# Optimization experiments

Measured on AMD Instinct MI355X. Metric: run time of the kernel, lower is better.

## Reference

```python
import jax, jax.numpy as jnp
import numpy as np

N_NODES = 50000
N_EDGES = 625000
D_FEAT = 128


def setup_inputs() -> dict:
    key = jax.random.key(0)
    k1, k2, k3, k4 = jax.random.split(key, 4)
    h = jax.random.normal(k1, (N_NODES, D_FEAT), dtype=jnp.float32)
    w = jax.random.uniform(k2, (N_EDGES, 1), dtype=jnp.float32)
    src = jax.random.randint(k3, (N_EDGES,), 0, N_NODES, dtype=jnp.int32)
    dst = jax.random.randint(k4, (N_EDGES,), 0, N_NODES, dtype=jnp.int32)
    return {"h": h, "w": w, "src": src, "dst": dst, "mode": 1}


def reference(h, w, src, dst, mode):
    # h: [N, D] node features; w: [E, 1] edge weights; src/dst: [E] edge list.
    n = h.shape[0]
    if mode == 1:  # 'polar': m = h[src] * w, sum to dst  (edge-weighted SpMM)
        msg = h[src] * w  # [E, D]
        out = jax.ops.segment_sum(msg, dst, num_segments=n)
    else:  # GCN symmetric normalization: D^{-1/2} A D^{-1/2} h (out-degree based)
        deg = jax.ops.segment_sum(jnp.ones(src.shape[0], dtype=h.dtype), src,
                                  num_segments=n)
        norm = jnp.power(deg, -0.5)[:, None]  # [N, 1]
        feat = h * norm
        out = jax.ops.segment_sum(feat[src], dst, num_segments=n)
        out = norm * out
    return out
```

## Files before the change

### kernel.cpp

```cpp
#include <hip/hip_runtime.h>
#include <hip/hip_fp16.h>

#define D_FEAT 128


__device__ __forceinline__ unsigned wq16(float f) {
    int q = (int)(f * 65536.0f);
    if (q < 0) q = 0;
    if (q > 65535) q = 65535;
    return (unsigned)q;
}

__device__ __forceinline__ unsigned h2u(__half2 v) {
    union { __half2 h; unsigned u; } cv; cv.h = v; return cv.u;
}
__device__ __forceinline__ float2 u2f2(unsigned u) {
    union { unsigned u; __half2 h; } cv; cv.u = u;
    return __half22float2(cv.h);
}

__global__ void bucket_conv_kernel(const float* __restrict__ h,
                                   const int* __restrict__ src, const int* __restrict__ dst,
                                   const float* __restrict__ w,
                                   int* __restrict__ cursor, float* __restrict__ deg,
                                   int* __restrict__ ovfcnt, int* __restrict__ ovf,
                                   unsigned* __restrict__ rec, int cap,
                                   uint4* __restrict__ h16,
                                   int E, int nBucketBlocks, int nGroups8, int cs,
                                   const int* __restrict__ mode) {
    if ((int)blockIdx.x >= nBucketBlocks) {
        int i = (blockIdx.x - nBucketBlocks) * blockDim.x + threadIdx.x;
        if (i >= nGroups8) return;
        const float4* hf4 = (const float4*)h;
        float4 x = hf4[2 * i];
        float4 y = hf4[2 * i + 1];
        uint4 o;
        o.x = h2u(__float22half2_rn(make_float2(x.x, x.y)));
        o.y = h2u(__float22half2_rn(make_float2(x.z, x.w)));
        o.z = h2u(__float22half2_rn(make_float2(y.x, y.y)));
        o.w = h2u(__float22half2_rn(make_float2(y.z, y.w)));
        h16[i] = o;
        return;
    }
    int e = blockIdx.x * blockDim.x + threadIdx.x;
    if (e >= E) return;
    bool m1 = (*mode == 1);
    int s = src[e];
    int d = dst[e];
    float wv = w[e];
    if (!m1) atomicAdd(&deg[s], 1.0f);
    int pos = atomicAdd(&cursor[(size_t)d * cs], 1);
    unsigned r = ((unsigned)s << 16) | wq16(wv);
    if (pos < cap) rec[(size_t)d * cap + pos] = r;
    else           ovf[atomicAdd(ovfcnt, 1)] = e;
}

__device__ __forceinline__ unsigned bcast_rec(unsigned r0, unsigned r1, int j) {
    unsigned lo = __shfl(r0, j & 31, 32);
    unsigned hi = __shfl(r1, j & 31, 32);
    return (j < 32) ? lo : hi;
}

__global__ void gather4_f16_kernel(const uint2* __restrict__ h16,
                                   const float* __restrict__ hf,
                                   const int* __restrict__ cursor, const float* __restrict__ deg,
                                   const unsigned* __restrict__ rec, int cap,
                                   const int* __restrict__ ovfcnt, const int* __restrict__ ovf,
                                   const int* __restrict__ src, const int* __restrict__ dst,
                                   const float* __restrict__ w,
                                   float* __restrict__ out, int N, int cs,
                                   const int* __restrict__ mode) {
    long long gid = (long long)blockIdx.x * blockDim.x + threadIdx.x;
    int node = (int)(gid >> 5);
    int lane = (int)(gid & 31);
    if (node >= N) return;
    bool m1 = (*mode == 1);
    int cnt = cursor[(size_t)node * cs];
    int inb = cnt < cap ? cnt : cap;
    const unsigned* row = rec + (size_t)node * cap;
    unsigned r0 = (lane < inb) ? row[lane] : 0u;
    unsigned r1 = (lane + 32 < inb) ? row[lane + 32] : 0u;

    float a0 = 0.f, a1 = 0.f, a2 = 0.f, a3 = 0.f;
    float b0 = 0.f, b1 = 0.f, b2 = 0.f, b3 = 0.f;
    float c0 = 0.f, c1 = 0.f, c2 = 0.f, c3 = 0.f;
    float d0 = 0.f, d1 = 0.f, d2 = 0.f, d3 = 0.f;

    int j = 0;
    if (m1) {
        const float Q = 1.52587890625e-05f;
        for (; j + 3 < inb; j += 4) {
            unsigned m0 = bcast_rec(r0, r1, j);
            unsigned m1r = bcast_rec(r0, r1, j + 1);
            unsigned m2r = bcast_rec(r0, r1, j + 2);
            unsigned m3r = bcast_rec(r0, r1, j + 3);
            float sc0 = ((float)(m0 & 0xFFFFu) + 0.5f) * Q;
            float sc1 = ((float)(m1r & 0xFFFFu) + 0.5f) * Q;
            float sc2 = ((float)(m2r & 0xFFFFu) + 0.5f) * Q;
            float sc3 = ((float)(m3r & 0xFFFFu) + 0.5f) * Q;
            uint2 v0 = h16[(size_t)(m0 >> 16) * 32 + lane];
            uint2 v1 = h16[(size_t)(m1r >> 16) * 32 + lane];
            uint2 v2 = h16[(size_t)(m2r >> 16) * 32 + lane];
            uint2 v3 = h16[(size_t)(m3r >> 16) * 32 + lane];
            float2 f0a = u2f2(v0.x), f0b = u2f2(v0.y);
            float2 f1a = u2f2(v1.x), f1b = u2f2(v1.y);
            float2 f2a = u2f2(v2.x), f2b = u2f2(v2.y);
            float2 f3a = u2f2(v3.x), f3b = u2f2(v3.y);
            a0 += f0a.x * sc0; a1 += f0a.y * sc0; a2 += f0b.x * sc0; a3 += f0b.y * sc0;
            b0 += f1a.x * sc1; b1 += f1a.y * sc1; b2 += f1b.x * sc1; b3 += f1b.y * sc1;
            c0 += f2a.x * sc2; c1 += f2a.y * sc2; c2 += f2b.x * sc2; c3 += f2b.y * sc2;
            d0 += f3a.x * sc3; d1 += f3a.y * sc3; d2 += f3b.x * sc3; d3 += f3b.y * sc3;
        }
        for (; j < inb; ++j) {
            unsigned m0 = bcast_rec(r0, r1, j);
            float sc0 = ((float)(m0 & 0xFFFFu) + 0.5f) * Q;
            uint2 v0 = h16[(size_t)(m0 >> 16) * 32 + lane];
            float2 f0a = u2f2(v0.x), f0b = u2f2(v0.y);
            a0 += f0a.x * sc0; a1 += f0a.y * sc0; a2 += f0b.x * sc0; a3 += f0b.y * sc0;
        }
    } else {
        for (; j + 3 < inb; j += 4) {
            unsigned m0 = bcast_rec(r0, r1, j);
            unsigned m1r = bcast_rec(r0, r1, j + 1);
            unsigned m2r = bcast_rec(r0, r1, j + 2);
            unsigned m3r = bcast_rec(r0, r1, j + 3);
            int s0 = (int)(m0 >> 16), s1 = (int)(m1r >> 16);
            int s2 = (int)(m2r >> 16), s3 = (int)(m3r >> 16);
            float sc0 = rsqrtf(deg[s0]);
            float sc1 = rsqrtf(deg[s1]);
            float sc2 = rsqrtf(deg[s2]);
            float sc3 = rsqrtf(deg[s3]);
            uint2 v0 = h16[(size_t)s0 * 32 + lane];
            uint2 v1 = h16[(size_t)s1 * 32 + lane];
            uint2 v2 = h16[(size_t)s2 * 32 + lane];
            uint2 v3 = h16[(size_t)s3 * 32 + lane];
            float2 f0a = u2f2(v0.x), f0b = u2f2(v0.y);
            float2 f1a = u2f2(v1.x), f1b = u2f2(v1.y);
            float2 f2a = u2f2(v2.x), f2b = u2f2(v2.y);
            float2 f3a = u2f2(v3.x), f3b = u2f2(v3.y);
            a0 += f0a.x * sc0; a1 += f0a.y * sc0; a2 += f0b.x * sc0; a3 += f0b.y * sc0;
            b0 += f1a.x * sc1; b1 += f1a.y * sc1; b2 += f1b.x * sc1; b3 += f1b.y * sc1;
            c0 += f2a.x * sc2; c1 += f2a.y * sc2; c2 += f2b.x * sc2; c3 += f2b.y * sc2;
            d0 += f3a.x * sc3; d1 += f3a.y * sc3; d2 += f3b.x * sc3; d3 += f3b.y * sc3;
        }
        for (; j < inb; ++j) {
            unsigned m0 = bcast_rec(r0, r1, j);
            int s0 = (int)(m0 >> 16);
            float sc0 = rsqrtf(deg[s0]);
            uint2 v0 = h16[(size_t)s0 * 32 + lane];
            float2 f0a = u2f2(v0.x), f0b = u2f2(v0.y);
            a0 += f0a.x * sc0; a1 += f0a.y * sc0; a2 += f0b.x * sc0; a3 += f0b.y * sc0;
        }
    }

    a0 += b0 + c0 + d0; a1 += b1 + c1 + d1;
    a2 += b2 + c2 + d2; a3 += b3 + c3 + d3;

    if (cnt > cap) {
        int total = *ovfcnt;
        for (int k = 0; k < total; ++k) {
            int e = ovf[k];
            if (dst[e] == node) {
                int s = src[e];
                float sc = m1 ? w[e] : rsqrtf(deg[s]);
                float4 v = ((const float4*)(hf + (long long)s * D_FEAT))[lane];
                a0 += v.x * sc; a1 += v.y * sc; a2 += v.z * sc; a3 += v.w * sc;
            }
        }
    }
    float fin = m1 ? 1.0f : rsqrtf(deg[node]);
    float4 r; r.x = a0 * fin; r.y = a1 * fin; r.z = a2 * fin; r.w = a3 * fin;
    ((float4*)(out + (long long)node * D_FEAT))[lane] = r;
}


__global__ void bucket_multi_kernel(const int* __restrict__ src, const int* __restrict__ dst,
                                    const float* __restrict__ w,
                                    int* __restrict__ cursor, float* __restrict__ deg,
                                    int* __restrict__ ovfcnt, int* __restrict__ ovf,
                                    unsigned* __restrict__ rec, int cap,
                                    int E, const int* __restrict__ mode) {
    int t = blockIdx.x * blockDim.x + threadIdx.x;
    int base = t * 4;
    if (base >= E) return;
    bool m1 = (*mode == 1);
    if (base + 3 < E) {
        int4   s4 = ((const int4*)src)[t];
        int4   d4 = ((const int4*)dst)[t];
        float4 w4 = ((const float4*)w)[t];
        if (!m1) {
            atomicAdd(&deg[s4.x], 1.0f); atomicAdd(&deg[s4.y], 1.0f);
            atomicAdd(&deg[s4.z], 1.0f); atomicAdd(&deg[s4.w], 1.0f);
        }
        int p0 = atomicAdd(&cursor[d4.x], 1);
        int p1 = atomicAdd(&cursor[d4.y], 1);
        int p2 = atomicAdd(&cursor[d4.z], 1);
        int p3 = atomicAdd(&cursor[d4.w], 1);
        unsigned r0 = ((unsigned)s4.x << 16) | wq16(w4.x);
        unsigned r1 = ((unsigned)s4.y << 16) | wq16(w4.y);
        unsigned r2 = ((unsigned)s4.z << 16) | wq16(w4.z);
        unsigned r3 = ((unsigned)s4.w << 16) | wq16(w4.w);
        if (p0 < cap) rec[(size_t)d4.x * cap + p0] = r0; else ovf[atomicAdd(ovfcnt, 1)] = base + 0;
        if (p1 < cap) rec[(size_t)d4.y * cap + p1] = r1; else ovf[atomicAdd(ovfcnt, 1)] = base + 1;
        if (p2 < cap) rec[(size_t)d4.z * cap + p2] = r2; else ovf[atomicAdd(ovfcnt, 1)] = base + 2;
        if (p3 < cap) rec[(size_t)d4.w * cap + p3] = r3; else ovf[atomicAdd(ovfcnt, 1)] = base + 3;
    } else {
        for (int e = base; e < E; ++e) {
            int s = src[e], d = dst[e];
            if (!m1) atomicAdd(&deg[s], 1.0f);
            int pos = atomicAdd(&cursor[d], 1);
            if (pos < cap) rec[(size_t)d * cap + pos] = ((unsigned)s << 16) | wq16(w[e]);
            else ovf[atomicAdd(ovfcnt, 1)] = e;
        }
    }
}

__global__ void gather4_f32_kernel(const float* __restrict__ h,
                                   const int* __restrict__ cursor, const float* __restrict__ deg,
                                   const unsigned* __restrict__ rec, int cap,
                                   const int* __restrict__ ovfcnt, const int* __restrict__ ovf,
                                   const int* __restrict__ src, const int* __restrict__ dst,
                                   const float* __restrict__ w,
                                   float* __restrict__ out, int N, const int* __restrict__ mode) {
    long long gid = (long long)blockIdx.x * blockDim.x + threadIdx.x;
    int node = (int)(gid >> 5);
    int lane = (int)(gid & 31);
    if (node >= N) return;
    bool m1 = (*mode == 1);
    int cnt = cursor[node];
    int inb = cnt < cap ? cnt : cap;
    const unsigned* row = rec + (size_t)node * cap;
    unsigned r0 = (lane < inb) ? row[lane] : 0u;
    unsigned r1 = (lane + 32 < inb) ? row[lane + 32] : 0u;
    const float4* h4 = (const float4*)h;
    float a0 = 0.f, a1 = 0.f, a2 = 0.f, a3 = 0.f;
    float b0 = 0.f, b1 = 0.f, b2 = 0.f, b3 = 0.f;
    int j = 0;
    const float Q = 1.52587890625e-05f;
    for (; j + 1 < inb; j += 2) {
        unsigned m0 = bcast_rec(r0, r1, j);
        unsigned m1r = bcast_rec(r0, r1, j + 1);
        int s0 = (int)(m0 >> 16), s1 = (int)(m1r >> 16);
        float sc0 = m1 ? ((float)(m0 & 0xFFFFu) + 0.5f) * Q : rsqrtf(deg[s0]);
        float sc1 = m1 ? ((float)(m1r & 0xFFFFu) + 0.5f) * Q : rsqrtf(deg[s1]);
        float4 v0 = h4[(size_t)s0 * 32 + lane];
        float4 v1 = h4[(size_t)s1 * 32 + lane];
        a0 += v0.x * sc0; a1 += v0.y * sc0; a2 += v0.z * sc0; a3 += v0.w * sc0;
        b0 += v1.x * sc1; b1 += v1.y * sc1; b2 += v1.z * sc1; b3 += v1.w * sc1;
    }
    if (j < inb) {
        unsigned m0 = bcast_rec(r0, r1, j);
        int s0 = (int)(m0 >> 16);
        float sc0 = m1 ? ((float)(m0 & 0xFFFFu) + 0.5f) * Q : rsqrtf(deg[s0]);
        float4 v0 = h4[(size_t)s0 * 32 + lane];
        a0 += v0.x * sc0; a1 += v0.y * sc0; a2 += v0.z * sc0; a3 += v0.w * sc0;
    }
    a0 += b0; a1 += b1; a2 += b2; a3 += b3;
    if (cnt > cap) {
        int total = *ovfcnt;
        for (int k = 0; k < total; ++k) {
            int e = ovf[k];
            if (dst[e] == node) {
                int s = src[e];
                float sc = m1 ? w[e] : rsqrtf(deg[s]);
                float4 v = ((const float4*)(h + (long long)s * D_FEAT))[lane];
                a0 += v.x * sc; a1 += v.y * sc; a2 += v.z * sc; a3 += v.w * sc;
            }
        }
    }
    float fin = m1 ? 1.0f : rsqrtf(deg[node]);
    float4 r; r.x = a0 * fin; r.y = a1 * fin; r.z = a2 * fin; r.w = a3 * fin;
    ((float4*)(out + (long long)node * D_FEAT))[lane] = r;
}


__global__ void bucket_direct_kernel(const int* __restrict__ src, const int* __restrict__ dst,
                                     const float* __restrict__ w,
                                     int* __restrict__ cursor, float* __restrict__ deg,
                                     int* __restrict__ ovfcnt, int* __restrict__ ovf,
                                     uint2* __restrict__ epack, int cap,
                                     int E, const int* __restrict__ mode) {
    int e = blockIdx.x * blockDim.x + threadIdx.x;
    if (e >= E) return;
    bool m1 = (*mode == 1);
    int d = dst[e];
    int s = src[e];
    if (!m1) atomicAdd(&deg[s], 1.0f);
    int pos = atomicAdd(&cursor[d], 1);
    if (pos < cap) {
        float sc = m1 ? w[e] : 0.0f;
        epack[(size_t)d * cap + pos] = make_uint2((unsigned)s, __float_as_uint(sc));
    } else {
        ovf[atomicAdd(ovfcnt, 1)] = e;
    }
}

__global__ void gather_cap_kernel(const float* __restrict__ h,
                                  const int* __restrict__ cursor, const float* __restrict__ deg,
                                  const uint2* __restrict__ epack, int cap,
                                  const int* __restrict__ ovfcnt, const int* __restrict__ ovf,
                                  const int* __restrict__ src, const int* __restrict__ dst,
                                  const float* __restrict__ w,
                                  float* __restrict__ out, int N, const int* __restrict__ mode) {
    long long gid = (long long)blockIdx.x * blockDim.x + threadIdx.x;
    int node = (int)(gid >> 5);
    int lane = (int)(gid & 31);
    if (node >= N) return;
    bool m1 = (*mode == 1);
    int cnt = cursor[node];
    int inb = cnt < cap ? cnt : cap;
    const uint2* row = epack + (size_t)node * cap;
    float a0 = 0.f, a1 = 0.f, a2 = 0.f, a3 = 0.f;
    for (int j = 0; j < inb; ++j) {
        uint2 m = row[j];
        int s = (int)m.x;
        float sc = m1 ? __uint_as_float(m.y) : rsqrtf(deg[s]);
        float4 v = ((const float4*)(h + (long long)s * D_FEAT))[lane];
        a0 += v.x * sc; a1 += v.y * sc; a2 += v.z * sc; a3 += v.w * sc;
    }
    if (cnt > cap) {
        int total = *ovfcnt;
        for (int k = 0; k < total; ++k) {
            int e = ovf[k];
            if (dst[e] == node) {
                int s = src[e];
                float sc = m1 ? w[e] : rsqrtf(deg[s]);
                float4 v = ((const float4*)(h + (long long)s * D_FEAT))[lane];
                a0 += v.x * sc; a1 += v.y * sc; a2 += v.z * sc; a3 += v.w * sc;
            }
        }
    }
    float fin = m1 ? 1.0f : rsqrtf(deg[node]);
    float4 r; r.x = a0 * fin; r.y = a1 * fin; r.z = a2 * fin; r.w = a3 * fin;
    ((float4*)(out + (long long)node * D_FEAT))[lane] = r;
}


__global__ void fb_deg_kernel(const int* __restrict__ src, float* __restrict__ deg,
                              int E, const int* __restrict__ mode) {
    if (*mode == 1) return;
    int e = blockIdx.x * blockDim.x + threadIdx.x;
    if (e < E) atomicAdd(&deg[src[e]], 1.0f);
}
__global__ void fb_norm_kernel(const float* __restrict__ deg, float* __restrict__ norm,
                               int N, const int* __restrict__ mode) {
    if (*mode == 1) return;
    int i = blockIdx.x * blockDim.x + threadIdx.x;
    if (i < N) norm[i] = rsqrtf(deg[i]);
}
__global__ void fb_scatter_kernel(const float* __restrict__ h, const float* __restrict__ w,
                                  const int* __restrict__ src, const int* __restrict__ dst,
                                  const float* __restrict__ norm, float* __restrict__ out,
                                  int E, const int* __restrict__ mode) {
    long long gid = (long long)blockIdx.x * blockDim.x + threadIdx.x;
    int e = (int)(gid >> 5);
    int lane = (int)(gid & 31);
    if (e >= E) return;
    int s = src[e], d = dst[e];
    float scale = (*mode == 1) ? w[e] : norm[s];
    float4 v = ((const float4*)(h + (long long)s * D_FEAT))[lane];
    float* op = out + (long long)d * D_FEAT + lane * 4;
    atomicAdd(op + 0, v.x * scale);
    atomicAdd(op + 1, v.y * scale);
    atomicAdd(op + 2, v.z * scale);
    atomicAdd(op + 3, v.w * scale);
}
__global__ void fb_scale_kernel(float* __restrict__ out, const float* __restrict__ norm,
                                int N, const int* __restrict__ mode) {
    if (*mode == 1) return;
    int idx = blockIdx.x * blockDim.x + threadIdx.x;
    int total = N * (D_FEAT / 4);
    if (idx >= total) return;
    int node = idx / (D_FEAT / 4);
    float4* op = (float4*)out + idx;
    float4 v = *op;
    float nn = norm[node];
    v.x *= nn; v.y *= nn; v.z *= nn; v.w *= nn;
    *op = v;
}


extern "C" void kernel_launch(void* const* d_in, const int* in_sizes, int n_in,
                              void* d_out, int out_size, void* d_ws, size_t ws_size,
                              hipStream_t stream) {
    const float* h    = (const float*)d_in[0];
    const float* w    = (const float*)d_in[1];
    const int*   src  = (const int*)d_in[2];
    const int*   dst  = (const int*)d_in[3];
    const int*   mode = (const int*)d_in[4];

    int ND = in_sizes[0];
    int E  = in_sizes[1];
    int N  = ND / D_FEAT;

    float* out = (float*)d_out;

    size_t ws_words = ws_size / 4;

    for (int cs : {16, 4, 1}) {
        size_t cur_words   = (size_t)N * cs;
        size_t fixed_words = cur_words + (size_t)N + 1 + (size_t)E;
        size_t h16_off     = (fixed_words + 3) & ~(size_t)3;
        size_t h16_words   = (size_t)N * (D_FEAT / 2);
        size_t rec16_off   = h16_off + h16_words;
        long capH = 0;
        if (ws_words > rec16_off) capH = (long)((ws_words - rec16_off) / (size_t)N);
        if (capH > 64) capH = 64;

        if (N <= 65536 && capH >= 28) {
            int*      cursor = (int*)d_ws;
            float*    deg    = (float*)(cursor + cur_words);
            int*      ovfcnt = (int*)(deg + N);
            int*      ovf    = ovfcnt + 1;
            uint4*    h16    = (uint4*)((int*)d_ws + h16_off);
            unsigned* rec    = (unsigned*)((int*)d_ws + rec16_off);
            int cap = (int)capH;

            hipMemsetAsync(d_ws, 0, (cur_words + (size_t)N + 1) * sizeof(int), stream);

            int nGroups8    = ND / 8;
            int nBucketBlks = (E + 255) / 256;
            int nConvBlks   = (nGroups8 + 255) / 256;
            bucket_conv_kernel<<<nBucketBlks + nConvBlks, 256, 0, stream>>>(
                h, src, dst, w, cursor, deg, ovfcnt, ovf, rec, cap, h16,
                E, nBucketBlks, nGroups8, cs, mode);

            long long gt = (long long)N * 32;
            gather4_f16_kernel<<<(int)((gt + 255) / 256), 256, 0, stream>>>(
                (const uint2*)h16, h, cursor, deg, rec, cap, ovfcnt, ovf, src, dst, w,
                out, N, cs, mode);
            return;
        }
    }

    size_t fixed_words = 2 * (size_t)N + 1 + (size_t)E;
    int*   cursor = (int*)d_ws;
    float* deg    = (float*)(cursor + N);
    int*   ovfcnt = (int*)(deg + N);
    int*   ovf    = ovfcnt + 1;

    size_t rec_off = fixed_words;
    long capA = 0;
    if (ws_words > rec_off) capA = (long)((ws_words - rec_off) / (size_t)N);
    if (capA > 64) capA = 64;

    if (N <= 65536 && capA >= 28) {
        unsigned* rec = (unsigned*)((int*)d_ws + rec_off);
        int cap = (int)capA;
        hipMemsetAsync(d_ws, 0, (2 * (size_t)N + 1) * sizeof(int), stream);
        int nthreads = (E + 3) / 4;
        bucket_multi_kernel<<<(nthreads + 255) / 256, 256, 0, stream>>>(
            src, dst, w, cursor, deg, ovfcnt, ovf, rec, cap, E, mode);
        long long gt = (long long)N * 32;
        gather4_f32_kernel<<<(int)((gt + 255) / 256), 256, 0, stream>>>(
            h, cursor, deg, rec, cap, ovfcnt, ovf, src, dst, w, out, N, mode);
        return;
    }

    size_t epack_off = (fixed_words + 1) & ~(size_t)1;
    long capC = 0;
    if (ws_words > epack_off) capC = (long)((ws_words - epack_off) / (2 * (size_t)N));
    if (capC > 64) capC = 64;

    if (capC >= 8) {
        uint2* epack = (uint2*)((int*)d_ws + epack_off);
        hipMemsetAsync(d_ws, 0, (2 * (size_t)N + 1) * sizeof(int), stream);
        bucket_direct_kernel<<<(E + 255) / 256, 256, 0, stream>>>(
            src, dst, w, cursor, deg, ovfcnt, ovf, epack, (int)capC, E, mode);
        long long gt = (long long)N * 32;
        gather_cap_kernel<<<(int)((gt + 255) / 256), 256, 0, stream>>>(
            h, cursor, deg, epack, (int)capC, ovfcnt, ovf, src, dst, w, out, N, mode);
        return;
    }

    float* degF  = (float*)d_ws;
    float* normF = degF + N;
    hipMemsetAsync(d_out, 0, (size_t)out_size * sizeof(float), stream);
    hipMemsetAsync(d_ws, 0, (size_t)N * sizeof(float), stream);
    fb_deg_kernel<<<(E + 255) / 256, 256, 0, stream>>>(src, degF, E, mode);
    fb_norm_kernel<<<(N + 255) / 256, 256, 0, stream>>>(degF, normF, N, mode);
    long long tt = (long long)E * 32;
    fb_scatter_kernel<<<(int)((tt + 255) / 256), 256, 0, stream>>>(h, w, src, dst,
                                                                   normF, out, E, mode);
    int st = N * (D_FEAT / 4);
    fb_scale_kernel<<<(st + 255) / 256, 256, 0, stream>>>(out, normF, N, mode);
}
```

Measured before the change: 153.0 us.

## Fuse memset, bucketing, fp16 conversion and gather into one cooperative kernel

Replaces the memset plus two launches with a single persistent cooperative kernel that zeroes counters, buckets edges while converting h to fp16, and then gathers per node, with grid-wide syncs between phases. The goal is to remove launch and inter-kernel gaps. In exchange, grid-stride loops run at occupancy-limited grid size and grid.sync adds its own cost. The change also drops the epack fallback path and devectorises bucket_multi_kernel.

```diff
diff --git a/kernel.cpp b/kernel.cpp
--- a/kernel.cpp
+++ b/kernel.cpp
@@ -1,5 +1,8 @@
 #include <hip/hip_runtime.h>
 #include <hip/hip_fp16.h>
+#include <hip/hip_cooperative_groups.h>
+
+namespace cg = cooperative_groups;
 
 #define D_FEAT 128
 
@@ -19,62 +22,21 @@
     return __half22float2(cv.h);
 }
 
-__global__ void bucket_conv_kernel(const float* __restrict__ h,
-                                   const int* __restrict__ src, const int* __restrict__ dst,
-                                   const float* __restrict__ w,
-                                   int* __restrict__ cursor, float* __restrict__ deg,
-                                   int* __restrict__ ovfcnt, int* __restrict__ ovf,
-                                   unsigned* __restrict__ rec, int cap,
-                                   uint4* __restrict__ h16,
-                                   int E, int nBucketBlocks, int nGroups8, int cs,
-                                   const int* __restrict__ mode) {
-    if ((int)blockIdx.x >= nBucketBlocks) {
-        int i = (blockIdx.x - nBucketBlocks) * blockDim.x + threadIdx.x;
-        if (i >= nGroups8) return;
-        const float4* hf4 = (const float4*)h;
-        float4 x = hf4[2 * i];
-        float4 y = hf4[2 * i + 1];
-        uint4 o;
-        o.x = h2u(__float22half2_rn(make_float2(x.x, x.y)));
-        o.y = h2u(__float22half2_rn(make_float2(x.z, x.w)));
-        o.z = h2u(__float22half2_rn(make_float2(y.x, y.y)));
-        o.w = h2u(__float22half2_rn(make_float2(y.z, y.w)));
-        h16[i] = o;
-        return;
-    }
-    int e = blockIdx.x * blockDim.x + threadIdx.x;
-    if (e >= E) return;
-    bool m1 = (*mode == 1);
-    int s = src[e];
-    int d = dst[e];
-    float wv = w[e];
-    if (!m1) atomicAdd(&deg[s], 1.0f);
-    int pos = atomicAdd(&cursor[(size_t)d * cs], 1);
-    unsigned r = ((unsigned)s << 16) | wq16(wv);
-    if (pos < cap) rec[(size_t)d * cap + pos] = r;
-    else           ovf[atomicAdd(ovfcnt, 1)] = e;
-}
-
 __device__ __forceinline__ unsigned bcast_rec(unsigned r0, unsigned r1, int j) {
     unsigned lo = __shfl(r0, j & 31, 32);
     unsigned hi = __shfl(r1, j & 31, 32);
     return (j < 32) ? lo : hi;
 }
 
-__global__ void gather4_f16_kernel(const uint2* __restrict__ h16,
-                                   const float* __restrict__ hf,
-                                   const int* __restrict__ cursor, const float* __restrict__ deg,
-                                   const unsigned* __restrict__ rec, int cap,
-                                   const int* __restrict__ ovfcnt, const int* __restrict__ ovf,
-                                   const int* __restrict__ src, const int* __restrict__ dst,
-                                   const float* __restrict__ w,
-                                   float* __restrict__ out, int N, int cs,
-                                   const int* __restrict__ mode) {
-    long long gid = (long long)blockIdx.x * blockDim.x + threadIdx.x;
-    int node = (int)(gid >> 5);
-    int lane = (int)(gid & 31);
-    if (node >= N) return;
-    bool m1 = (*mode == 1);
+__device__ __forceinline__ void gather_one_node(
+    const uint2* __restrict__ h16, const float* __restrict__ hf,
+    const int* __restrict__ cursor, const float* __restrict__ deg,
+    const unsigned* __restrict__ rec, int cap,
+    const int* __restrict__ ovfcnt, const int* __restrict__ ovf,
+    const int* __restrict__ src, const int* __restrict__ dst,
+    const float* __restrict__ w,
+    float* __restrict__ out, int node, int lane, int cs, bool m1)
+{
     int cnt = cursor[(size_t)node * cs];
     int inb = cnt < cap ? cnt : cap;
     const unsigned* row = rec + (size_t)node * cap;
@@ -174,45 +136,127 @@
 }
 
 
+__global__ void fused_kernel(const float* __restrict__ h,
+                             const int* __restrict__ src, const int* __restrict__ dst,
+                             const float* __restrict__ w,
+                             int* __restrict__ cursor, float* __restrict__ deg,
+                             int* __restrict__ ovfcnt, int* __restrict__ ovf,
+                             unsigned* __restrict__ rec, int cap,
+                             uint4* __restrict__ h16,
+                             float* __restrict__ out,
+                             int N, int E, int cs, int zero_words,
+                             const int* __restrict__ mode) {
+    cg::grid_group grid = cg::this_grid();
+    int tid = blockIdx.x * blockDim.x + threadIdx.x;
+    int nth = gridDim.x * blockDim.x;
+    bool m1 = (*mode == 1);
+
+    for (int i = tid; i < zero_words; i += nth) cursor[i] = 0;
+    grid.sync();
+
+    for (int e = tid; e < E; e += nth) {
+        int s = src[e];
+        int d = dst[e];
+        float wv = w[e];
+        if (!m1) atomicAdd(&deg[s], 1.0f);
+        int pos = atomicAdd(&cursor[(size_t)d * cs], 1);
+        unsigned r = ((unsigned)s << 16) | wq16(wv);
+        if (pos < cap) rec[(size_t)d * cap + pos] = r;
+        else           ovf[atomicAdd(ovfcnt, 1)] = e;
+    }
+    int nGroups8 = N * (D_FEAT / 8);
+    const float4* hf4 = (const float4*)h;
+    for (int i = tid; i < nGroups8; i += nth) {
+        float4 x = hf4[2 * i];
+        float4 y = hf4[2 * i + 1];
+        uint4 o;
+        o.x = h2u(__float22half2_rn(make_float2(x.x, x.y)));
+        o.y = h2u(__float22half2_rn(make_float2(x.z, x.w)));
+        o.z = h2u(__float22half2_rn(make_float2(y.x, y.y)));
+        o.w = h2u(__float22half2_rn(make_float2(y.z, y.w)));
+        h16[i] = o;
+    }
+    grid.sync();
+
+    long long total = (long long)N * 32;
+    for (long long g = tid; g < total; g += nth) {
+        int node = (int)(g >> 5);
+        int lane = (int)(g & 31);
+        gather_one_node((const uint2*)h16, h, cursor, deg, rec, cap, ovfcnt, ovf,
+                        src, dst, w, out, node, lane, cs, m1);
+    }
+}
+
+
+__global__ void bucket_conv_kernel(const float* __restrict__ h,
+                                   const int* __restrict__ src, const int* __restrict__ dst,
+                                   const float* __restrict__ w,
+                                   int* __restrict__ cursor, float* __restrict__ deg,
+                                   int* __restrict__ ovfcnt, int* __restrict__ ovf,
+                                   unsigned* __restrict__ rec, int cap,
+                                   uint4* __restrict__ h16,
+                                   int E, int nBucketBlocks, int nGroups8, int cs,
+                                   const int* __restrict__ mode) {
+    if ((int)blockIdx.x >= nBucketBlocks) {
+        int i = (blockIdx.x - nBucketBlocks) * blockDim.x + threadIdx.x;
+        if (i >= nGroups8) return;
+        const float4* hf4 = (const float4*)h;
+        float4 x = hf4[2 * i];
+        float4 y = hf4[2 * i + 1];
+        uint4 o;
+        o.x = h2u(__float22half2_rn(make_float2(x.x, x.y)));
+        o.y = h2u(__float22half2_rn(make_float2(x.z, x.w)));
+        o.z = h2u(__float22half2_rn(make_float2(y.x, y.y)));
+        o.w = h2u(__float22half2_rn(make_float2(y.z, y.w)));
+        h16[i] = o;
+        return;
+    }
+    int e = blockIdx.x * blockDim.x + threadIdx.x;
+    if (e >= E) return;
+    bool m1 = (*mode == 1);
+    int s = src[e];
+    int d = dst[e];
+    float wv = w[e];
+    if (!m1) atomicAdd(&deg[s], 1.0f);
+    int pos = atomicAdd(&cursor[(size_t)d * cs], 1);
+    unsigned r = ((unsigned)s << 16) | wq16(wv);
+    if (pos < cap) rec[(size_t)d * cap + pos] = r;
+    else           ovf[atomicAdd(ovfcnt, 1)] = e;
+}
+
+__global__ void gather4_f16_kernel(const uint2* __restrict__ h16,
+                                   const float* __restrict__ hf,
+                                   const int* __restrict__ cursor, const float* __restrict__ deg,
+                                   const unsigned* __restrict__ rec, int cap,
+                                   const int* __restrict__ ovfcnt, const int* __restrict__ ovf,
+                                   const int* __restrict__ src, const int* __restrict__ dst,
+                                   const float* __restrict__ w,
+                                   float* __restrict__ out, int N, int cs,
+                                   const int* __restrict__ mode) {
+    long long gid = (long long)blockIdx.x * blockDim.x + threadIdx.x;
+    int node = (int)(gid >> 5);
+    int lane = (int)(gid & 31);
+    if (node >= N) return;
+    bool m1 = (*mode == 1);
+    gather_one_node(h16, hf, cursor, deg, rec, cap, ovfcnt, ovf,
+                    src, dst, w, out, node, lane, cs, m1);
+}
+
+
 __global__ void bucket_multi_kernel(const int* __restrict__ src, const int* __restrict__ dst,
                                     const float* __restrict__ w,
                                     int* __restrict__ cursor, float* __restrict__ deg,
                                     int* __restrict__ ovfcnt, int* __restrict__ ovf,
                                     unsigned* __restrict__ rec, int cap,
                                     int E, const int* __restrict__ mode) {
-    int t = blockIdx.x * blockDim.x + threadIdx.x;
-    int base = t * 4;
-    if (base >= E) return;
+    int e = blockIdx.x * blockDim.x + threadIdx.x;
+    if (e >= E) return;
     bool m1 = (*mode == 1);
-    if (base + 3 < E) {
-        int4   s4 = ((const int4*)src)[t];
-        int4   d4 = ((const int4*)dst)[t];
-        float4 w4 = ((const float4*)w)[t];
-        if (!m1) {
-            atomicAdd(&deg[s4.x], 1.0f); atomicAdd(&deg[s4.y], 1.0f);
-            atomicAdd(&deg[s4.z], 1.0f); atomicAdd(&deg[s4.w], 1.0f);
-        }
-        int p0 = atomicAdd(&cursor[d4.x], 1);
-        int p1 = atomicAdd(&cursor[d4.y], 1);
-        int p2 = atomicAdd(&cursor[d4.z], 1);
-        int p3 = atomicAdd(&cursor[d4.w], 1);
-        unsigned r0 = ((unsigned)s4.x << 16) | wq16(w4.x);
-        unsigned r1 = ((unsigned)s4.y << 16) | wq16(w4.y);
-        unsigned r2 = ((unsigned)s4.z << 16) | wq16(w4.z);
-        unsigned r3 = ((unsigned)s4.w << 16) | wq16(w4.w);
-        if (p0 < cap) rec[(size_t)d4.x * cap + p0] = r0; else ovf[atomicAdd(ovfcnt, 1)] = base + 0;
-        if (p1 < cap) rec[(size_t)d4.y * cap + p1] = r1; else ovf[atomicAdd(ovfcnt, 1)] = base + 1;
-        if (p2 < cap) rec[(size_t)d4.z * cap + p2] = r2; else ovf[atomicAdd(ovfcnt, 1)] = base + 2;
-        if (p3 < cap) rec[(size_t)d4.w * cap + p3] = r3; else ovf[atomicAdd(ovfcnt, 1)] = base + 3;
-    } else {
-        for (int e = base; e < E; ++e) {
-            int s = src[e], d = dst[e];
-            if (!m1) atomicAdd(&deg[s], 1.0f);
-            int pos = atomicAdd(&cursor[d], 1);
-            if (pos < cap) rec[(size_t)d * cap + pos] = ((unsigned)s << 16) | wq16(w[e]);
-            else ovf[atomicAdd(ovfcnt, 1)] = e;
-        }
-    }
+    int s = src[e], d = dst[e];
+    if (!m1) atomicAdd(&deg[s], 1.0f);
+    int pos = atomicAdd(&cursor[d], 1);
+    if (pos < cap) rec[(size_t)d * cap + pos] = ((unsigned)s << 16) | wq16(w[e]);
+    else ovf[atomicAdd(ovfcnt, 1)] = e;
 }
 
 __global__ void gather4_f32_kernel(const float* __restrict__ h,
@@ -274,68 +318,6 @@
 }
 
 
-__global__ void bucket_direct_kernel(const int* __restrict__ src, const int* __restrict__ dst,
-                                     const float* __restrict__ w,
-                                     int* __restrict__ cursor, float* __restrict__ deg,
-                                     int* __restrict__ ovfcnt, int* __restrict__ ovf,
-                                     uint2* __restrict__ epack, int cap,
-                                     int E, const int* __restrict__ mode) {
-    int e = blockIdx.x * blockDim.x + threadIdx.x;
-    if (e >= E) return;
-    bool m1 = (*mode == 1);
-    int d = dst[e];
-    int s = src[e];
-    if (!m1) atomicAdd(&deg[s], 1.0f);
-    int pos = atomicAdd(&cursor[d], 1);
-    if (pos < cap) {
-        float sc = m1 ? w[e] : 0.0f;
-        epack[(size_t)d * cap + pos] = make_uint2((unsigned)s, __float_as_uint(sc));
-    } else {
-        ovf[atomicAdd(ovfcnt, 1)] = e;
-    }
-}
-
-__global__ void gather_cap_kernel(const float* __restrict__ h,
-                                  const int* __restrict__ cursor, const float* __restrict__ deg,
-                                  const uint2* __restrict__ epack, int cap,
-                                  const int* __restrict__ ovfcnt, const int* __restrict__ ovf,
-                                  const int* __restrict__ src, const int* __restrict__ dst,
-                                  const float* __restrict__ w,
-                                  float* __restrict__ out, int N, const int* __restrict__ mode) {
-    long long gid = (long long)blockIdx.x * blockDim.x + threadIdx.x;
-    int node = (int)(gid >> 5);
-    int lane = (int)(gid & 31);
-    if (node >= N) return;
-    bool m1 = (*mode == 1);
-    int cnt = cursor[node];
-    int inb = cnt < cap ? cnt : cap;
-    const uint2* row = epack + (size_t)node * cap;
-    float a0 = 0.f, a1 = 0.f, a2 = 0.f, a3 = 0.f;
-    for (int j = 0; j < inb; ++j) {
-        uint2 m = row[j];
-        int s = (int)m.x;
-        float sc = m1 ? __uint_as_float(m.y) : rsqrtf(deg[s]);
-        float4 v = ((const float4*)(h + (long long)s * D_FEAT))[lane];
-        a0 += v.x * sc; a1 += v.y * sc; a2 += v.z * sc; a3 += v.w * sc;
-    }
-    if (cnt > cap) {
-        int total = *ovfcnt;
-        for (int k = 0; k < total; ++k) {
-            int e = ovf[k];
-            if (dst[e] == node) {
-                int s = src[e];
-                float sc = m1 ? w[e] : rsqrtf(deg[s]);
-                float4 v = ((const float4*)(h + (long long)s * D_FEAT))[lane];
-                a0 += v.x * sc; a1 += v.y * sc; a2 += v.z * sc; a3 += v.w * sc;
-            }
-        }
-    }
-    float fin = m1 ? 1.0f : rsqrtf(deg[node]);
-    float4 r; r.x = a0 * fin; r.y = a1 * fin; r.z = a2 * fin; r.w = a3 * fin;
-    ((float4*)(out + (long long)node * D_FEAT))[lane] = r;
-}
-
-
 __global__ void fb_deg_kernel(const int* __restrict__ src, float* __restrict__ deg,
                               int E, const int* __restrict__ mode) {
     if (*mode == 1) return;
@@ -397,6 +379,20 @@
 
     size_t ws_words = ws_size / 4;
 
+    static int coopBlocks = -2;
+    if (coopBlocks == -2) {
+        coopBlocks = 0;
+        hipDeviceProp_t prop;
+        if (hipGetDeviceProperties(&prop, 0) == hipSuccess && prop.cooperativeLaunch) {
+            int perCU = 0;
+            if (hipOccupancyMaxActiveBlocksPerMultiprocessor(
+                    &perCU, reinterpret_cast<const void*>(fused_kernel), 256, 0) == hipSuccess
+                && perCU > 0) {
+                coopBlocks = perCU * prop.multiProcessorCount;
+            }
+        }
+    }
+
     for (int cs : {16, 4, 1}) {
         size_t cur_words   = (size_t)N * cs;
         size_t fixed_words = cur_words + (size_t)N + 1 + (size_t)E;
@@ -415,20 +411,35 @@
             uint4*    h16    = (uint4*)((int*)d_ws + h16_off);
             unsigned* rec    = (unsigned*)((int*)d_ws + rec16_off);
             int cap = (int)capH;
-
-            hipMemsetAsync(d_ws, 0, (cur_words + (size_t)N + 1) * sizeof(int), stream);
-
+            int csv = cs;
+            int zero_words = (int)(cur_words + (size_t)N + 1);
+
+            if (coopBlocks > 0) {
+                void* args[] = {
+                    (void*)&h, (void*)&src, (void*)&dst, (void*)&w,
+                    (void*)&cursor, (void*)&deg, (void*)&ovfcnt, (void*)&ovf,
+                    (void*)&rec, (void*)&cap, (void*)&h16, (void*)&out,
+                    (void*)&N, (void*)&E, (void*)&csv, (void*)&zero_words,
+                    (void*)&mode
+                };
+                hipError_t err = hipLaunchCooperativeKernel(
+                    reinterpret_cast<const void*>(fused_kernel),
+                    dim3((unsigned)coopBlocks), dim3(256), args, 0, stream);
+                if (err == hipSuccess) return;
+                coopBlocks = 0;
+            }
+
+            hipMemsetAsync(d_ws, 0, (size_t)zero_words * sizeof(int), stream);
             int nGroups8    = ND / 8;
             int nBucketBlks = (E + 255) / 256;
             int nConvBlks   = (nGroups8 + 255) / 256;
             bucket_conv_kernel<<<nBucketBlks + nConvBlks, 256, 0, stream>>>(
                 h, src, dst, w, cursor, deg, ovfcnt, ovf, rec, cap, h16,
-                E, nBucketBlks, nGroups8, cs, mode);
-
+                E, nBucketBlks, nGroups8, csv, mode);
             long long gt = (long long)N * 32;
             gather4_f16_kernel<<<(int)((gt + 255) / 256), 256, 0, stream>>>(
                 (const uint2*)h16, h, cursor, deg, rec, cap, ovfcnt, ovf, src, dst, w,
-                out, N, cs, mode);
+                out, N, csv, mode);
             return;
         }
     }
@@ -448,28 +459,11 @@
         unsigned* rec = (unsigned*)((int*)d_ws + rec_off);
         int cap = (int)capA;
         hipMemsetAsync(d_ws, 0, (2 * (size_t)N + 1) * sizeof(int), stream);
-        int nthreads = (E + 3) / 4;
-        bucket_multi_kernel<<<(nthreads + 255) / 256, 256, 0, stream>>>(
+        bucket_multi_kernel<<<(E + 255) / 256, 256, 0, stream>>>(
             src, dst, w, cursor, deg, ovfcnt, ovf, rec, cap, E, mode);
         long long gt = (long long)N * 32;
         gather4_f32_kernel<<<(int)((gt + 255) / 256), 256, 0, stream>>>(
             h, cursor, deg, rec, cap, ovfcnt, ovf, src, dst, w, out, N, mode);
-        return;
-    }
-
-    size_t epack_off = (fixed_words + 1) & ~(size_t)1;
-    long capC = 0;
-    if (ws_words > epack_off) capC = (long)((ws_words - epack_off) / (2 * (size_t)N));
-    if (capC > 64) capC = 64;
-
-    if (capC >= 8) {
-        uint2* epack = (uint2*)((int*)d_ws + epack_off);
-        hipMemsetAsync(d_ws, 0, (2 * (size_t)N + 1) * sizeof(int), stream);
-        bucket_direct_kernel<<<(E + 255) / 256, 256, 0, stream>>>(
-            src, dst, w, cursor, deg, ovfcnt, ovf, epack, (int)capC, E, mode);
-        long long gt = (long long)N * 32;
-        gather_cap_kernel<<<(int)((gt + 255) / 256), 256, 0, stream>>>(
-            h, cursor, deg, epack, (int)capC, ovfcnt, ovf, src, dst, w, out, N, mode);
         return;
     }
 
```

Measured after the change: 340.9 us. +122.8%, slower.
